# Optimization experiments

Hardware: AMD Instinct MI355X
Metric: run time of the kernel (lower is better)

The kernel has to match this reference:

```python
import jax, jax.numpy as jnp
import numpy as np

HID, HEADS, DH, L = 64, 8, 8, 2  # hidden_dim, num_heads, head_dim, num_layers


def setup_inputs() -> dict:
    key = jax.random.key(0)
    ks = jax.random.split(key, 18)
    B, S, N, Cin, Cout, E = 4, 12, 512, 3, 3, 8192
    p = lambda k, shape: (jax.random.normal(k, shape, jnp.float32) * 0.05)
    return {
        "x": jax.random.normal(ks[0], (B, S, N, Cin), jnp.float32),
        "edge_index": jax.random.randint(ks[1], (2, E), 0, N),
        "Win": p(ks[2], (HID, Cin)), "b_in": p(ks[3], (HID,)),
        "Wqs": p(ks[4], (L, HID, HID)), "bqs": p(ks[5], (L, HID)),
        "Wks": p(ks[6], (L, HID, HID)), "bks": p(ks[7], (L, HID)),
        "Wvs": p(ks[8], (L, HID, HID)), "bvs": p(ks[9], (L, HID)),
        "Wqt": p(ks[10], (L, HID, HID)), "bqt": p(ks[11], (L, HID)),
        "Wkt": p(ks[12], (L, HID, HID)), "bkt": p(ks[13], (L, HID)),
        "Wvt": p(ks[14], (L, HID, HID)), "bvt": p(ks[15], (L, HID)),
        "Wout": p(ks[16], (Cout, HID)), "bout": p(ks[17], (Cout,)),
    }


def reference(x, edge_index, Win, b_in, Wqs, bqs, Wks, bks, Wvs, bvs,
              Wqt, bqt, Wkt, bkt, Wvt, bvt, Wout, bout):
    B, S, N, _ = x.shape
    scale = 1.0 / np.sqrt(DH).astype(np.float32)
    # input projection: [B,S,N,Cin] -> [B,S,N,HID]
    h = x @ Win.T + b_in
    # dense NxN edge mask, exactly as the torch module builds it
    mask = jnp.zeros((N, N), jnp.float32).at[edge_index[0], edge_index[1]].set(1.0)
    for l in range(L):
        # ---- spatial attention (over nodes, per (batch, time)) ----
        q = (h @ Wqs[l].T + bqs[l]).reshape(B, S, N, HEADS, DH)
        k = (h @ Wks[l].T + bks[l]).reshape(B, S, N, HEADS, DH)
        v = (h @ Wvs[l].T + bvs[l]).reshape(B, S, N, HEADS, DH)
        s = jnp.einsum('bsnhd,bsmhd->bshnm', q, k) * scale  # [B,S,H,N,N]
        s = jnp.where(mask[None, None, None] == 0, jnp.float32(-1e9), s)
        a = jax.nn.softmax(s, axis=-1)
        h = jnp.einsum('bshnm,bsmhd->bsnhd', a, v).reshape(B, S, N, HID)
        # ---- temporal attention (over seq, per (batch, node)) ----
        q = (h @ Wqt[l].T + bqt[l]).reshape(B, S, N, HEADS, DH)
        k = (h @ Wkt[l].T + bkt[l]).reshape(B, S, N, HEADS, DH)
        v = (h @ Wvt[l].T + bvt[l]).reshape(B, S, N, HEADS, DH)
        s = jnp.einsum('bsnhd,btnhd->bnhst', q, k) * scale  # [B,N,H,S,S]
        a = jax.nn.softmax(s, axis=-1)
        h = jnp.einsum('bnhst,btnhd->bsnhd', a, v).reshape(B, S, N, HID)
    # take last time step, project to out_channels
    return h[:, -1] @ Wout.T + bout
```

## Files before the change

### kernel.cpp

```cpp
#include <hip/hip_runtime.h>
#include <hip/hip_bf16.h>

#define HIDN   64
#define NHEADS 8
#define DHEAD  8
#define NLAY   2
#define BB     4
#define SS     12
#define NNODE  512
#define NEDGE  8192
#define XELEMS (BB * SS * NNODE * 3)
#define ROWS   (BB * SS * NNODE)
#define QSCALE 0.51006967f

typedef unsigned short u16;
typedef unsigned int   u32;
typedef __attribute__((ext_vector_type(4))) float f4;
typedef __attribute__((ext_vector_type(8))) short s8v;

__device__ __forceinline__ float b2f(u16 u) {
    union { u32 i; float f; } c; c.i = ((u32)u) << 16; return c.f;
}
__device__ __forceinline__ u16 f2b(float f) {
    union { float f; u32 i; } c; c.f = f;
    u32 r = c.i + 0x7FFFu + ((c.i >> 16) & 1u);
    return (u16)(r >> 16);
}
__device__ __forceinline__ u32 pk2(float a, float b) {
    return (u32)f2b(a) | ((u32)f2b(b) << 16);
}
__device__ __forceinline__ float ld(const void* p, int i, int fl) {
    return fl ? ((const float*)p)[i] : b2f(((const u16*)p)[i]);
}

__global__ void detect_kernel(const u16* __restrict__ x, int* __restrict__ flag) {
    int i0 = blockIdx.x * 256 + threadIdx.x;
    int bad = 0;
    for (int i = i0; i < XELEMS; i += 64 * 256) {
        float v = fabsf(b2f(x[i]));
        if (!(v <= 100.f)) bad = 1;
    }
    if (bad) atomicOr(flag, 1);
}

struct PrepArgs {
    const void* x; const void* Win; const void* bin; u16* h;
    const void* Wq[2]; const void* bq[2];
    const void* Wk[2]; const void* bk[2];
    const void* Wv[2]; const void* bv[2];
    u16* wb; u16* whd; float* bp[2];
    const int* ei; int* row_ptr; u16* col_idx;
};
__global__ __launch_bounds__(512) void prep_kernel(PrepArgs a, const int* __restrict__ flagp,
                                                   int flv) {
    __shared__ u32 msk[NNODE * 16];
    __shared__ int sc[512];
    int fl = (flv >= 0) ? flv : (*flagp != 0);
    int bid = blockIdx.x;
    int tid = threadIdx.x;
    if (bid < 384) {
        int base = (bid * 512 + tid) * 8;
        int row = base >> 6, j0 = base & 63;
        float x0 = ld(a.x, row * 3, fl);
        float x1 = ld(a.x, row * 3 + 1, fl);
        float x2 = ld(a.x, row * 3 + 2, fl);
        float o[8];
#pragma unroll
        for (int jj = 0; jj < 8; ++jj) {
            int j = j0 + jj;
            o[jj] = ld(a.bin, j, fl) + x0 * ld(a.Win, j * 3, fl)
                  + x1 * ld(a.Win, j * 3 + 1, fl) + x2 * ld(a.Win, j * 3 + 2, fl);
        }
        *(uint4*)&a.h[base] = make_uint4(pk2(o[0], o[1]), pk2(o[2], o[3]),
                                         pk2(o[4], o[5]), pk2(o[6], o[7]));
        return;
    }
    if (bid < 432) {
        int u = (bid - 384) * 512 + tid;
        int l = u / 12288;
        int t = u - l * 12288;
        int j = t >> 6, i = t & 63;
        int cg = j >> 6, cc = j & 63;
        const void* W = (cg == 0) ? a.Wq[1] : (cg == 1) ? a.Wk[1] : a.Wv[1];
        a.wb[u] = f2b(ld(W, l * 4096 + cc * 64 + i, fl));
        if (u < 768) {
            int p2 = u / 384;
            int r3 = u - p2 * 384;
            int l2 = r3 / 192;
            int j2 = r3 - l2 * 192;
            int cg2 = j2 >> 6;
            const void* B = (cg2 == 0) ? a.bq[p2] : (cg2 == 1) ? a.bk[p2] : a.bv[p2];
            a.bp[p2][l2 * 192 + j2] = ld(B, l2 * 64 + (j2 & 63), fl);
        }
        return;
    }
    if (bid < 496) {
        int u = (bid - 432) * 512 + tid;
        int l    = u >> 14;
        int rem  = u & 16383;
        int hd   = rem >> 11;
        int rem2 = rem & 2047;
        int tile = rem2 >> 10;
        int rem3 = rem2 & 1023;
        int c    = rem3 >> 6;
        int i    = rem3 & 63;
        int j;
        if (tile == 0) j = (c < 8) ? (64 + hd * 8 + c) : (128 + hd * 8 + (c - 8));
        else           j = (c < 8) ? (hd * 8 + c) : -1;
        u16 val = 0;
        if (j >= 0) {
            int cg = j >> 6, cc = j & 63;
            const void* W = (cg == 0) ? a.Wq[0] : (cg == 1) ? a.Wk[0] : a.Wv[0];
            val = f2b(ld(W, l * 4096 + cc * 64 + i, fl));
        }
        a.whd[u] = val;
        return;
    }
    for (int i = tid; i < NNODE * 16; i += 512) msk[i] = 0;
    __syncthreads();
    for (int e = tid; e < NEDGE; e += 512) {
        int r = a.ei[e];
        int m = a.ei[NEDGE + e];
        atomicOr(&msk[r * 16 + (m >> 5)], 1u << (m & 31));
    }
    __syncthreads();
    int n = tid;
    u32 w[16];
    int d = 0;
#pragma unroll
    for (int i = 0; i < 16; ++i) { w[i] = msk[n * 16 + i]; d += __popc(w[i]); }
    sc[n] = d;
    __syncthreads();
    for (int s = 1; s < 512; s <<= 1) {
        int v = (n >= s) ? sc[n - s] : 0;
        __syncthreads();
        sc[n] += v;
        __syncthreads();
    }
    int excl = sc[n] - d;
    a.row_ptr[n] = excl;
    if (n == 511) a.row_ptr[512] = sc[511];
    int base = excl;
#pragma unroll
    for (int i = 0; i < 16; ++i) {
        u32 m = w[i];
        while (m) {
            int b = __ffs(m) - 1;
            m &= m - 1;
            a.col_idx[base++] = (u16)(i * 32 + b);
        }
    }
}

__global__ __launch_bounds__(512) void spat_fused_kernel(
    const u16* __restrict__ hb, const u16* __restrict__ whd,
    const float* __restrict__ bp,
    const int* __restrict__ row_ptr, const u16* __restrict__ col_idx,
    u16* __restrict__ h2) {
    __shared__ __align__(16) float Ks[NNODE][8];
    __shared__ __align__(16) float Vs[NNODE][8];
    __shared__ float qS[NNODE][9];
    int pair = blockIdx.x;
    int bs = pair >> 3, hd = pair & 7;
    int t = threadIdx.x;
    int lane = t & 63, wv = t >> 6;
    int lrow = lane & 15, kg = lane >> 4;
    const u16* hsl = hb + (long)bs * NNODE * HIDN;
    const u16* wkv = whd + hd * 2048;
    const u16* wq  = whd + hd * 2048 + 1024;
    s8v bkv0 = *(const s8v*)(wkv + lrow * 64 + kg * 8);
    s8v bkv1 = *(const s8v*)(wkv + lrow * 64 + kg * 8 + 32);
    s8v bq0  = *(const s8v*)(wq  + lrow * 64 + kg * 8);
    s8v bq1  = *(const s8v*)(wq  + lrow * 64 + kg * 8 + 32);
    float biasKV = (lrow < 8) ? bp[64 + hd * 8 + lrow] : bp[128 + hd * 8 + (lrow & 7)];
    float biasQ  = bp[hd * 8 + (lrow & 7)];
#pragma unroll
    for (int s = 0; s < 4; ++s) {
        int rt = wv * 4 + s;
        const u16* ap = hsl + (rt * 16 + lrow) * 64 + kg * 8;
        s8v ha0 = *(const s8v*)ap;
        s8v ha1 = *(const s8v*)(ap + 32);
        f4 acc = (f4){0.f, 0.f, 0.f, 0.f};
        acc = __builtin_amdgcn_mfma_f32_16x16x32_bf16(ha0, bkv0, acc, 0, 0, 0);
        acc = __builtin_amdgcn_mfma_f32_16x16x32_bf16(ha1, bkv1, acc, 0, 0, 0);
        int node = rt * 16 + kg * 4;
        if (lrow < 8) {
#pragma unroll
            for (int r = 0; r < 4; ++r) Ks[node + r][lrow] = acc[r] + biasKV;
        } else {
#pragma unroll
            for (int r = 0; r < 4; ++r) Vs[node + r][lrow & 7] = acc[r] + biasKV;
        }
    }
#pragma unroll
    for (int s = 0; s < 4; ++s) {
        int rt = wv * 4 + s;
        const u16* ap = hsl + (rt * 16 + lrow) * 64 + kg * 8;
        s8v ha0 = *(const s8v*)ap;
        s8v ha1 = *(const s8v*)(ap + 32);
        f4 acc = (f4){0.f, 0.f, 0.f, 0.f};
        acc = __builtin_amdgcn_mfma_f32_16x16x32_bf16(ha0, bq0, acc, 0, 0, 0);
        acc = __builtin_amdgcn_mfma_f32_16x16x32_bf16(ha1, bq1, acc, 0, 0, 0);
        if (lrow < 8) {
            int nl = rt * 16 + kg * 4;
#pragma unroll
            for (int r = 0; r < 4; ++r) qS[nl + r][lrow] = (acc[r] + biasQ) * QSCALE;
        }
    }
    __syncthreads();
    int n = t;
    float4 qa = make_float4(qS[n][0], qS[n][1], qS[n][2], qS[n][3]);
    float4 qc = make_float4(qS[n][4], qS[n][5], qS[n][6], qS[n][7]);
    int e0 = row_ptr[n], e1 = row_ptr[n + 1];
    float l = 0.f;
    float o0=0.f,o1=0.f,o2=0.f,o3=0.f,o4=0.f,o5=0.f,o6=0.f,o7=0.f;
    for (int e = e0; e < e1; ++e) {
        int m = col_idx[e];
        float4 ka = *(const float4*)&Ks[m][0];
        float4 kc = *(const float4*)&Ks[m][4];
        float s = qa.x*ka.x + qa.y*ka.y + qa.z*ka.z + qa.w*ka.w
                + qc.x*kc.x + qc.y*kc.y + qc.z*kc.z + qc.w*kc.w;
        float p = exp2f(s);
        l += p;
        float4 va = *(const float4*)&Vs[m][0];
        float4 vc = *(const float4*)&Vs[m][4];
        o0 += p*va.x; o1 += p*va.y; o2 += p*va.z; o3 += p*va.w;
        o4 += p*vc.x; o5 += p*vc.y; o6 += p*vc.z; o7 += p*vc.w;
    }
    if (e1 == e0) {
        for (int m = 0; m < NNODE; ++m) {
            o0 += Vs[m][0]; o1 += Vs[m][1]; o2 += Vs[m][2]; o3 += Vs[m][3];
            o4 += Vs[m][4]; o5 += Vs[m][5]; o6 += Vs[m][6]; o7 += Vs[m][7];
        }
        l = (float)NNODE;
    }
    float inv = 1.f / l;
    u16* op = h2 + ((long)(bs * NNODE + n)) * HIDN + hd * 8;
    *(uint4*)op = make_uint4(pk2(o0*inv, o1*inv), pk2(o2*inv, o3*inv),
                             pk2(o4*inv, o5*inv), pk2(o6*inv, o7*inv));
}

__global__ __launch_bounds__(384) void temp_fused_kernel(
    const u16* __restrict__ h2b, const u16* __restrict__ wb,
    const float* __restrict__ bp, u16* __restrict__ h,
    const void* __restrict__ Wout, const void* __restrict__ bout,
    void* __restrict__ out, const int* __restrict__ flagp, int flv, int last) {
    __shared__ float S[3][SS][32][9];
    __shared__ u32 outS[4][32];
    int b  = blockIdx.x >> 7;
    int n0 = (blockIdx.x & 127) * 4;
    int t = threadIdx.x;
    int lane = t & 63, wv = t >> 6;
    int lrow = lane & 15, kg = lane >> 4;
    int rt  = wv >> 1;
    int ct0 = (wv & 1) * 6;
    int gr = rt * 16 + lrow;
    int tta = gr >> 2, nla = gr & 3;
    const u16* ap = h2b + ((long)((b * SS + tta) * NNODE) + n0 + nla) * HIDN + kg * 8;
    s8v haf0 = *(const s8v*)ap;
    s8v haf1 = *(const s8v*)(ap + 32);
#pragma unroll
    for (int s = 0; s < 6; ++s) {
        int ct = ct0 + s;
        const u16* wp = wb + (ct * 16 + lrow) * 64 + kg * 8;
        s8v wb0 = *(const s8v*)wp;
        s8v wb1 = *(const s8v*)(wp + 32);
        f4 acc = (f4){0.f, 0.f, 0.f, 0.f};
        acc = __builtin_amdgcn_mfma_f32_16x16x32_bf16(haf0, wb0, acc, 0, 0, 0);
        acc = __builtin_amdgcn_mfma_f32_16x16x32_bf16(haf1, wb1, acc, 0, 0, 0);
        int j = ct * 16 + lrow;
        float bb = bp[j];
        int tz = j >> 6, cc = j & 63, hd2 = cc >> 3, dh = cc & 7;
#pragma unroll
        for (int r = 0; r < 4; ++r) {
            int gr2 = rt * 16 + kg * 4 + r;
            S[tz][gr2 >> 2][(gr2 & 3) * 8 + hd2][dh] = acc[r] + bb;
        }
    }
    __syncthreads();
    int sq = t >> 5, r = t & 31;
    int nl = r >> 3, hd = r & 7;
    const float* qd = &S[0][sq][r][0];
    float q0=qd[0],q1=qd[1],q2=qd[2],q3=qd[3],q4=qd[4],q5=qd[5],q6=qd[6],q7=qd[7];
    float s[SS];
#pragma unroll
    for (int tt = 0; tt < SS; ++tt) {
        const float* kd = &S[1][tt][r][0];
        s[tt] = (q0 * kd[0] + q1 * kd[1] + q2 * kd[2] + q3 * kd[3] +
                 q4 * kd[4] + q5 * kd[5] + q6 * kd[6] + q7 * kd[7]) * QSCALE;
    }
    float mx = s[0];
#pragma unroll
    for (int tt = 1; tt < SS; ++tt) mx = fmaxf(mx, s[tt]);
    float l = 0.f;
#pragma unroll
    for (int tt = 0; tt < SS; ++tt) { s[tt] = exp2f(s[tt] - mx); l += s[tt]; }
    float a0=0.f,a1=0.f,a2=0.f,a3=0.f,a4=0.f,a5=0.f,a6=0.f,a7=0.f;
#pragma unroll
    for (int tt = 0; tt < SS; ++tt) {
        const float* vd = &S[2][tt][r][0];
        float e = s[tt];
        a0 += e * vd[0]; a1 += e * vd[1]; a2 += e * vd[2]; a3 += e * vd[3];
        a4 += e * vd[4]; a5 += e * vd[5]; a6 += e * vd[6]; a7 += e * vd[7];
    }
    float inv = 1.f / l;
    u32 p0 = pk2(a0*inv, a1*inv), p1 = pk2(a2*inv, a3*inv);
    u32 p2 = pk2(a4*inv, a5*inv), p3 = pk2(a6*inv, a7*inv);
    u16* op = h + ((long)((b * SS + sq) * NNODE) + n0 + nl) * HIDN + hd * 8;
    *(uint4*)op = make_uint4(p0, p1, p2, p3);
    if (last) {
        if (sq == SS - 1) {
            outS[nl][hd * 4 + 0] = p0;
            outS[nl][hd * 4 + 1] = p1;
            outS[nl][hd * 4 + 2] = p2;
            outS[nl][hd * 4 + 3] = p3;
        }
        __syncthreads();
        if (t < 12) {
            int fl = (flv >= 0) ? flv : (*flagp != 0);
            int c = t % 3, nl2 = t / 3;
            float acc = ld(bout, c, fl);
#pragma unroll
            for (int i = 0; i < HIDN; i += 8) {
                u32 hw0 = outS[nl2][i / 2 + 0];
                u32 hw1 = outS[nl2][i / 2 + 1];
                u32 hw2 = outS[nl2][i / 2 + 2];
                u32 hw3 = outS[nl2][i / 2 + 3];
                const u32 hw[4] = {hw0, hw1, hw2, hw3};
#pragma unroll
                for (int j2 = 0; j2 < 4; ++j2) {
                    float hlo = b2f((u16)(hw[j2] & 0xFFFF));
                    float hhi = b2f((u16)(hw[j2] >> 16));
                    acc += hlo * ld(Wout, c * 64 + i + j2 * 2,     fl)
                         + hhi * ld(Wout, c * 64 + i + j2 * 2 + 1, fl);
                }
            }
            int ti = (b * NNODE + n0 + nl2) * 3 + c;
            if (fl) ((float*)out)[ti] = acc;
            else    ((__hip_bfloat16*)out)[ti] = __float2bfloat16(acc);
        }
    }
}

extern "C" void kernel_launch(void* const* d_in, const int* in_sizes, int n_in,
                              void* d_out, int out_size, void* d_ws, size_t ws_size,
                              hipStream_t stream) {
    const int* ei = (const int*)d_in[1];

    float* ws = (float*)d_ws;
    int*   flag    = (int*)ws;
    int*   row_ptr = (int*)(ws + 64);
    u16*   col_idx = (u16*)(ws + 640);
    u16*   wb16  = (u16*)(ws + 4736);
    u16*   whd16 = (u16*)(ws + 4736 + 12288);
    float* bsp   = ws + 4736 + 12288 + 16384;
    float* btp   = bsp + 384;
    u16*   hb16  = (u16*)(btp + 384);
    u16*   h2b16 = hb16 + ROWS * HIDN;

    int flv = -1;
    if (in_sizes) {
        if (in_sizes[0] == XELEMS * 2) flv = 0;
        else if (in_sizes[0] == XELEMS * 4) flv = 1;
    }
    if (flv < 0) {
        (void)hipMemsetAsync(flag, 0, sizeof(int), stream);
        detect_kernel<<<64, 256, 0, stream>>>((const u16*)d_in[0], flag);
    }

    PrepArgs pr;
    pr.x = d_in[0]; pr.Win = d_in[2]; pr.bin = d_in[3]; pr.h = hb16;
    pr.Wq[0] = d_in[4];  pr.bq[0] = d_in[5];
    pr.Wk[0] = d_in[6];  pr.bk[0] = d_in[7];
    pr.Wv[0] = d_in[8];  pr.bv[0] = d_in[9];
    pr.Wq[1] = d_in[10]; pr.bq[1] = d_in[11];
    pr.Wk[1] = d_in[12]; pr.bk[1] = d_in[13];
    pr.Wv[1] = d_in[14]; pr.bv[1] = d_in[15];
    pr.wb = wb16; pr.whd = whd16; pr.bp[0] = bsp; pr.bp[1] = btp;
    pr.ei = ei; pr.row_ptr = row_ptr; pr.col_idx = col_idx;
    prep_kernel<<<384 + 48 + 64 + 1, 512, 0, stream>>>(pr, flag, flv);

    for (int l = 0; l < NLAY; ++l) {
        spat_fused_kernel<<<BB * SS * NHEADS, 512, 0, stream>>>(
            hb16, whd16 + l * 16384, bsp + l * 192, row_ptr, col_idx, h2b16);
        temp_fused_kernel<<<BB * (NNODE / 4), 384, 0, stream>>>(
            h2b16, wb16 + l * 12288, btp + l * 192, hb16,
            d_in[16], d_in[17], d_out, flag, flv, (l == NLAY - 1) ? 1 : 0);
    }
}
```

Before: 173.8 us.

## Fuse input projection and weight conversion into attention kernels, shrink prep to CSR

Drops the prep kernel's input-projection and weight-repacking stages. The first spatial layer now computes the input projection from x on the fly into its MFMA A-fragments. Both attention kernels load and convert weights and biases straight from the original inputs. The prep kernel becomes a single-block CSR builder, which removes a large hidden-state write and read plus extra prep work, at the cost of recomputing the projection in each of the 8 head blocks and doing per-block weight conversion loads.

```diff
diff --git a/kernel.cpp b/kernel.cpp
--- a/kernel.cpp
+++ b/kernel.cpp
@@ -32,6 +32,29 @@
 __device__ __forceinline__ float ld(const void* p, int i, int fl) {
     return fl ? ((const float*)p)[i] : b2f(((const u16*)p)[i]);
 }
+__device__ __forceinline__ s8v loadW(const void* W, int off, int fl) {
+    if (!fl) return *(const s8v*)((const u16*)W + off);
+    const float* wf = (const float*)W + off;
+    union { s8v v; uint4 u; } U;
+    U.u = make_uint4(pk2(wf[0], wf[1]), pk2(wf[2], wf[3]),
+                     pk2(wf[4], wf[5]), pk2(wf[6], wf[7]));
+    return U.v;
+}
+__device__ __forceinline__ s8v projfrag(float x0, float x1, float x2, int k0,
+                                        const float* WinS, const float* binS) {
+    u32 w[4];
+#pragma unroll
+    for (int p = 0; p < 4; ++p) {
+        int j = k0 + p * 2;
+        float h0 = binS[j]   + x0 * WinS[j * 3]       + x1 * WinS[j * 3 + 1]
+                             + x2 * WinS[j * 3 + 2];
+        float h1 = binS[j+1] + x0 * WinS[(j+1) * 3]   + x1 * WinS[(j+1) * 3 + 1]
+                             + x2 * WinS[(j+1) * 3 + 2];
+        w[p] = pk2(h0, h1);
+    }
+    union { s8v v; uint4 u; } U; U.u = make_uint4(w[0], w[1], w[2], w[3]);
+    return U.v;
+}
 
 __global__ void detect_kernel(const u16* __restrict__ x, int* __restrict__ flag) {
     int i0 = blockIdx.x * 256 + threadIdx.x;
@@ -43,84 +66,17 @@
     if (bad) atomicOr(flag, 1);
 }
 
-struct PrepArgs {
-    const void* x; const void* Win; const void* bin; u16* h;
-    const void* Wq[2]; const void* bq[2];
-    const void* Wk[2]; const void* bk[2];
-    const void* Wv[2]; const void* bv[2];
-    u16* wb; u16* whd; float* bp[2];
-    const int* ei; int* row_ptr; u16* col_idx;
-};
-__global__ __launch_bounds__(512) void prep_kernel(PrepArgs a, const int* __restrict__ flagp,
-                                                   int flv) {
+__global__ __launch_bounds__(512) void csr_kernel(const int* __restrict__ ei,
+                                                  int* __restrict__ row_ptr,
+                                                  u16* __restrict__ col_idx) {
     __shared__ u32 msk[NNODE * 16];
     __shared__ int sc[512];
-    int fl = (flv >= 0) ? flv : (*flagp != 0);
-    int bid = blockIdx.x;
     int tid = threadIdx.x;
-    if (bid < 384) {
-        int base = (bid * 512 + tid) * 8;
-        int row = base >> 6, j0 = base & 63;
-        float x0 = ld(a.x, row * 3, fl);
-        float x1 = ld(a.x, row * 3 + 1, fl);
-        float x2 = ld(a.x, row * 3 + 2, fl);
-        float o[8];
-#pragma unroll
-        for (int jj = 0; jj < 8; ++jj) {
-            int j = j0 + jj;
-            o[jj] = ld(a.bin, j, fl) + x0 * ld(a.Win, j * 3, fl)
-                  + x1 * ld(a.Win, j * 3 + 1, fl) + x2 * ld(a.Win, j * 3 + 2, fl);
-        }
-        *(uint4*)&a.h[base] = make_uint4(pk2(o[0], o[1]), pk2(o[2], o[3]),
-                                         pk2(o[4], o[5]), pk2(o[6], o[7]));
-        return;
-    }
-    if (bid < 432) {
-        int u = (bid - 384) * 512 + tid;
-        int l = u / 12288;
-        int t = u - l * 12288;
-        int j = t >> 6, i = t & 63;
-        int cg = j >> 6, cc = j & 63;
-        const void* W = (cg == 0) ? a.Wq[1] : (cg == 1) ? a.Wk[1] : a.Wv[1];
-        a.wb[u] = f2b(ld(W, l * 4096 + cc * 64 + i, fl));
-        if (u < 768) {
-            int p2 = u / 384;
-            int r3 = u - p2 * 384;
-            int l2 = r3 / 192;
-            int j2 = r3 - l2 * 192;
-            int cg2 = j2 >> 6;
-            const void* B = (cg2 == 0) ? a.bq[p2] : (cg2 == 1) ? a.bk[p2] : a.bv[p2];
-            a.bp[p2][l2 * 192 + j2] = ld(B, l2 * 64 + (j2 & 63), fl);
-        }
-        return;
-    }
-    if (bid < 496) {
-        int u = (bid - 432) * 512 + tid;
-        int l    = u >> 14;
-        int rem  = u & 16383;
-        int hd   = rem >> 11;
-        int rem2 = rem & 2047;
-        int tile = rem2 >> 10;
-        int rem3 = rem2 & 1023;
-        int c    = rem3 >> 6;
-        int i    = rem3 & 63;
-        int j;
-        if (tile == 0) j = (c < 8) ? (64 + hd * 8 + c) : (128 + hd * 8 + (c - 8));
-        else           j = (c < 8) ? (hd * 8 + c) : -1;
-        u16 val = 0;
-        if (j >= 0) {
-            int cg = j >> 6, cc = j & 63;
-            const void* W = (cg == 0) ? a.Wq[0] : (cg == 1) ? a.Wk[0] : a.Wv[0];
-            val = f2b(ld(W, l * 4096 + cc * 64 + i, fl));
-        }
-        a.whd[u] = val;
-        return;
-    }
     for (int i = tid; i < NNODE * 16; i += 512) msk[i] = 0;
     __syncthreads();
     for (int e = tid; e < NEDGE; e += 512) {
-        int r = a.ei[e];
-        int m = a.ei[NEDGE + e];
+        int r = ei[e];
+        int m = ei[NEDGE + e];
         atomicOr(&msk[r * 16 + (m >> 5)], 1u << (m & 31));
     }
     __syncthreads();
@@ -138,8 +94,8 @@
         __syncthreads();
     }
     int excl = sc[n] - d;
-    a.row_ptr[n] = excl;
-    if (n == 511) a.row_ptr[512] = sc[511];
+    row_ptr[n] = excl;
+    if (n == 511) row_ptr[512] = sc[511];
     int base = excl;
 #pragma unroll
     for (int i = 0; i < 16; ++i) {
@@ -147,39 +103,63 @@
         while (m) {
             int b = __ffs(m) - 1;
             m &= m - 1;
-            a.col_idx[base++] = (u16)(i * 32 + b);
+            col_idx[base++] = (u16)(i * 32 + b);
         }
     }
 }
 
 __global__ __launch_bounds__(512) void spat_fused_kernel(
-    const u16* __restrict__ hb, const u16* __restrict__ whd,
-    const float* __restrict__ bp,
+    const void* __restrict__ x, const u16* __restrict__ hb,
+    const void* __restrict__ Wq, const void* __restrict__ Wk, const void* __restrict__ Wv,
+    const void* __restrict__ bq, const void* __restrict__ bk, const void* __restrict__ bv,
+    const void* __restrict__ Win, const void* __restrict__ bin,
     const int* __restrict__ row_ptr, const u16* __restrict__ col_idx,
-    u16* __restrict__ h2) {
+    u16* __restrict__ h2, const int* __restrict__ flagp, int flv,
+    int loff4, int loff1, int lay0) {
     __shared__ __align__(16) float Ks[NNODE][8];
     __shared__ __align__(16) float Vs[NNODE][8];
     __shared__ float qS[NNODE][9];
+    __shared__ float WinS[192];
+    __shared__ float binS[64];
+    int fl = (flv >= 0) ? flv : (*flagp != 0);
     int pair = blockIdx.x;
     int bs = pair >> 3, hd = pair & 7;
     int t = threadIdx.x;
+    if (t < 192) WinS[t] = ld(Win, t, fl);
+    if (t < 64)  binS[t] = ld(bin, t, fl);
+    __syncthreads();
     int lane = t & 63, wv = t >> 6;
     int lrow = lane & 15, kg = lane >> 4;
     const u16* hsl = hb + (long)bs * NNODE * HIDN;
-    const u16* wkv = whd + hd * 2048;
-    const u16* wq  = whd + hd * 2048 + 1024;
-    s8v bkv0 = *(const s8v*)(wkv + lrow * 64 + kg * 8);
-    s8v bkv1 = *(const s8v*)(wkv + lrow * 64 + kg * 8 + 32);
-    s8v bq0  = *(const s8v*)(wq  + lrow * 64 + kg * 8);
-    s8v bq1  = *(const s8v*)(wq  + lrow * 64 + kg * 8 + 32);
-    float biasKV = (lrow < 8) ? bp[64 + hd * 8 + lrow] : bp[128 + hd * 8 + (lrow & 7)];
-    float biasQ  = bp[hd * 8 + (lrow & 7)];
+    int ccKV = hd * 8 + (lrow & 7);
+    const void* WKV = (lrow < 8) ? Wk : Wv;
+    s8v bkv0 = loadW(WKV, loff4 + ccKV * 64 + kg * 8,      fl);
+    s8v bkv1 = loadW(WKV, loff4 + ccKV * 64 + kg * 8 + 32, fl);
+    s8v bq0, bq1;
+    if (lrow < 8) {
+        bq0 = loadW(Wq, loff4 + ccKV * 64 + kg * 8,      fl);
+        bq1 = loadW(Wq, loff4 + ccKV * 64 + kg * 8 + 32, fl);
+    } else {
+        union { s8v v; uint4 u; } Z; Z.u = make_uint4(0, 0, 0, 0);
+        bq0 = Z.v; bq1 = Z.v;
+    }
+    float biasKV = (lrow < 8) ? ld(bk, loff1 + hd * 8 + lrow, fl)
+                              : ld(bv, loff1 + hd * 8 + (lrow & 7), fl);
+    float biasQ  = ld(bq, loff1 + hd * 8 + (lrow & 7), fl);
 #pragma unroll
     for (int s = 0; s < 4; ++s) {
         int rt = wv * 4 + s;
-        const u16* ap = hsl + (rt * 16 + lrow) * 64 + kg * 8;
-        s8v ha0 = *(const s8v*)ap;
-        s8v ha1 = *(const s8v*)(ap + 32);
+        s8v ha0, ha1;
+        if (lay0) {
+            long xr3 = ((long)bs * NNODE + rt * 16 + lrow) * 3;
+            float x0 = ld(x, xr3, fl), x1 = ld(x, xr3 + 1, fl), x2 = ld(x, xr3 + 2, fl);
+            ha0 = projfrag(x0, x1, x2, kg * 8,      WinS, binS);
+            ha1 = projfrag(x0, x1, x2, kg * 8 + 32, WinS, binS);
+        } else {
+            const u16* ap = hsl + (rt * 16 + lrow) * 64 + kg * 8;
+            ha0 = *(const s8v*)ap;
+            ha1 = *(const s8v*)(ap + 32);
+        }
         f4 acc = (f4){0.f, 0.f, 0.f, 0.f};
         acc = __builtin_amdgcn_mfma_f32_16x16x32_bf16(ha0, bkv0, acc, 0, 0, 0);
         acc = __builtin_amdgcn_mfma_f32_16x16x32_bf16(ha1, bkv1, acc, 0, 0, 0);
@@ -195,9 +175,17 @@
 #pragma unroll
     for (int s = 0; s < 4; ++s) {
         int rt = wv * 4 + s;
-        const u16* ap = hsl + (rt * 16 + lrow) * 64 + kg * 8;
-        s8v ha0 = *(const s8v*)ap;
-        s8v ha1 = *(const s8v*)(ap + 32);
+        s8v ha0, ha1;
+        if (lay0) {
+            long xr3 = ((long)bs * NNODE + rt * 16 + lrow) * 3;
+            float x0 = ld(x, xr3, fl), x1 = ld(x, xr3 + 1, fl), x2 = ld(x, xr3 + 2, fl);
+            ha0 = projfrag(x0, x1, x2, kg * 8,      WinS, binS);
+            ha1 = projfrag(x0, x1, x2, kg * 8 + 32, WinS, binS);
+        } else {
+            const u16* ap = hsl + (rt * 16 + lrow) * 64 + kg * 8;
+            ha0 = *(const s8v*)ap;
+            ha1 = *(const s8v*)(ap + 32);
+        }
         f4 acc = (f4){0.f, 0.f, 0.f, 0.f};
         acc = __builtin_amdgcn_mfma_f32_16x16x32_bf16(ha0, bq0, acc, 0, 0, 0);
         acc = __builtin_amdgcn_mfma_f32_16x16x32_bf16(ha1, bq1, acc, 0, 0, 0);
@@ -241,12 +229,16 @@
 }
 
 __global__ __launch_bounds__(384) void temp_fused_kernel(
-    const u16* __restrict__ h2b, const u16* __restrict__ wb,
-    const float* __restrict__ bp, u16* __restrict__ h,
+    const u16* __restrict__ h2b,
+    const void* __restrict__ Wq, const void* __restrict__ Wk, const void* __restrict__ Wv,
+    const void* __restrict__ bq, const void* __restrict__ bk, const void* __restrict__ bv,
+    u16* __restrict__ h,
     const void* __restrict__ Wout, const void* __restrict__ bout,
-    void* __restrict__ out, const int* __restrict__ flagp, int flv, int last) {
+    void* __restrict__ out, const int* __restrict__ flagp, int flv,
+    int loff4, int loff1, int last) {
     __shared__ float S[3][SS][32][9];
     __shared__ u32 outS[4][32];
+    int fl = (flv >= 0) ? flv : (*flagp != 0);
     int b  = blockIdx.x >> 7;
     int n0 = (blockIdx.x & 127) * 4;
     int t = threadIdx.x;
@@ -262,15 +254,16 @@
 #pragma unroll
     for (int s = 0; s < 6; ++s) {
         int ct = ct0 + s;
-        const u16* wp = wb + (ct * 16 + lrow) * 64 + kg * 8;
-        s8v wb0 = *(const s8v*)wp;
-        s8v wb1 = *(const s8v*)(wp + 32);
+        int j = ct * 16 + lrow;
+        int cg = j >> 6, cc = j & 63;
+        const void* W = (cg == 0) ? Wq : (cg == 1) ? Wk : Wv;
+        s8v wb0 = loadW(W, loff4 + cc * 64 + kg * 8,      fl);
+        s8v wb1 = loadW(W, loff4 + cc * 64 + kg * 8 + 32, fl);
         f4 acc = (f4){0.f, 0.f, 0.f, 0.f};
         acc = __builtin_amdgcn_mfma_f32_16x16x32_bf16(haf0, wb0, acc, 0, 0, 0);
         acc = __builtin_amdgcn_mfma_f32_16x16x32_bf16(haf1, wb1, acc, 0, 0, 0);
-        int j = ct * 16 + lrow;
-        float bb = bp[j];
-        int tz = j >> 6, cc = j & 63, hd2 = cc >> 3, dh = cc & 7;
+        float bb = ld((cg == 0) ? bq : (cg == 1) ? bk : bv, loff1 + cc, fl);
+        int tz = cg, hd2 = (cc >> 3), dh = cc & 7;
 #pragma unroll
         for (int r = 0; r < 4; ++r) {
             int gr2 = rt * 16 + kg * 4 + r;
@@ -317,7 +310,6 @@
         }
         __syncthreads();
         if (t < 12) {
-            int fl = (flv >= 0) ? flv : (*flagp != 0);
             int c = t % 3, nl2 = t / 3;
             float acc = ld(bout, c, fl);
 #pragma unroll
@@ -351,11 +343,7 @@
     int*   flag    = (int*)ws;
     int*   row_ptr = (int*)(ws + 64);
     u16*   col_idx = (u16*)(ws + 640);
-    u16*   wb16  = (u16*)(ws + 4736);
-    u16*   whd16 = (u16*)(ws + 4736 + 12288);
-    float* bsp   = ws + 4736 + 12288 + 16384;
-    float* btp   = bsp + 384;
-    u16*   hb16  = (u16*)(btp + 384);
+    u16*   hb16  = (u16*)(ws + 4736);
     u16*   h2b16 = hb16 + ROWS * HIDN;
 
     int flv = -1;
@@ -368,23 +356,23 @@
         detect_kernel<<<64, 256, 0, stream>>>((const u16*)d_in[0], flag);
     }
 
-    PrepArgs pr;
-    pr.x = d_in[0]; pr.Win = d_in[2]; pr.bin = d_in[3]; pr.h = hb16;
-    pr.Wq[0] = d_in[4];  pr.bq[0] = d_in[5];
-    pr.Wk[0] = d_in[6];  pr.bk[0] = d_in[7];
-    pr.Wv[0] = d_in[8];  pr.bv[0] = d_in[9];
-    pr.Wq[1] = d_in[10]; pr.bq[1] = d_in[11];
-    pr.Wk[1] = d_in[12]; pr.bk[1] = d_in[13];
-    pr.Wv[1] = d_in[14]; pr.bv[1] = d_in[15];
-    pr.wb = wb16; pr.whd = whd16; pr.bp[0] = bsp; pr.bp[1] = btp;
-    pr.ei = ei; pr.row_ptr = row_ptr; pr.col_idx = col_idx;
-    prep_kernel<<<384 + 48 + 64 + 1, 512, 0, stream>>>(pr, flag, flv);
+    csr_kernel<<<1, 512, 0, stream>>>(ei, row_ptr, col_idx);
 
     for (int l = 0; l < NLAY; ++l) {
         spat_fused_kernel<<<BB * SS * NHEADS, 512, 0, stream>>>(
-            hb16, whd16 + l * 16384, bsp + l * 192, row_ptr, col_idx, h2b16);
+            d_in[0], hb16,
+            d_in[4], d_in[6], d_in[8],
+            d_in[5], d_in[7], d_in[9],
+            d_in[2], d_in[3],
+            row_ptr, col_idx, h2b16, flag, flv,
+            l * 4096, l * 64, (l == 0) ? 1 : 0);
         temp_fused_kernel<<<BB * (NNODE / 4), 384, 0, stream>>>(
-            h2b16, wb16 + l * 12288, btp + l * 192, hb16,
-            d_in[16], d_in[17], d_out, flag, flv, (l == NLAY - 1) ? 1 : 0);
-    }
-}
+            h2b16,
+            d_in[10], d_in[12], d_in[14],
+            d_in[11], d_in[13], d_in[15],
+            hb16,
+            d_in[16], d_in[17],
+            d_out, flag, flv,
+            l * 4096, l * 64, (l == NLAY - 1) ? 1 : 0);
+    }
+}
```

Measured after the change: 186.6 us. +7.4%, slower.
